# Kernel optimization log

Hardware: AMD Instinct MI355X
Metric: run time of the kernel (lower is better)

Reference implementation:

```python
import jax, jax.numpy as jnp
import numpy as np

GAMMA = 0.5  # triplet_loss_gamma from __init__


def setup_inputs() -> dict:
    key = jax.random.key(0)
    k1, k2, k3 = jax.random.split(key, 3)
    b, n, m = 16, 2048, 2048
    scores = jax.random.normal(k1, (b, n + 1, m + 1), dtype=jnp.float32)
    gt_matches0 = jax.random.randint(k2, (b, n), 0, m, dtype=jnp.int32)
    gt_matches1 = jax.random.randint(k3, (b, m), 0, n, dtype=jnp.int32)
    return {"gt_matches0": gt_matches0, "gt_matches1": gt_matches1, "scores": scores}


def reference(gt_matches0, gt_matches1, scores):
    b, n = gt_matches0.shape
    m = gt_matches1.shape[1]
    # -1 means "unmatched" -> dustbin index (m for rows, n for cols)
    gt0 = jnp.where(gt_matches0 == -1, m, gt_matches0)
    gt1 = jnp.where(gt_matches1 == -1, n, gt_matches1)
    gamma_pos = jnp.maximum(jnp.float32(GAMMA), 0.0)  # clamp value at the matched slot

    # ---- anchor = rows (points in cloud 0) ----
    s0 = scores[:, :n, :]                                   # (b, n, m+1)
    pos0 = jnp.take_along_axis(s0, gt0[:, :, None], axis=2)  # (b, n, 1)
    # original computes -log(exp(pos)) - (-log(exp(neg))) + gamma == neg - pos + gamma
    gap0 = jnp.maximum(s0 - pos0 + GAMMA, 0.0)              # (b, n, m+1)
    # torch version excludes the matched column; its contribution is clamp(gamma, 0)
    sum0 = jnp.sum(gap0, axis=2) - gamma_pos                # (b, n)
    loss_mean = jnp.mean(2.0 * jnp.log(sum0 + 1.0), axis=1)  # (b,)

    # ---- anchor = columns (points in cloud 1) ----
    s1 = scores[:, :, :m]                                   # (b, n+1, m)
    pos1 = jnp.take_along_axis(s1, gt1[:, None, :], axis=1)  # (b, 1, m)
    gap1 = jnp.maximum(s1 - pos1 + GAMMA, 0.0)              # (b, n+1, m)
    sum1 = jnp.sum(gap1, axis=1) - gamma_pos                # (b, m)
    loss_mean2 = jnp.mean(2.0 * jnp.log(sum1 + 1.0), axis=1)  # (b,)

    return (loss_mean + loss_mean2) / 2.0
```

## Files before the change

kernel.cpp:

```cpp
#include <hip/hip_runtime.h>
#include <math.h>

#define BATCH 16
#define NN 2048
#define MM 2048
#define WW 2049
#define RPB 32
#define NCHUNK 65

__global__ __launch_bounds__(256) void gather_kernel(
    const float* __restrict__ scores, const int* __restrict__ gt0,
    const int* __restrict__ gt1, float* __restrict__ pos0, float* __restrict__ pos1)
{
    int id = blockIdx.x * 256 + threadIdx.x;
    const int half = BATCH * NN;
    if (id < half) {
        int b = id >> 11, i = id & (NN - 1);
        int g = gt0[id];
        g = (g == -1) ? MM : g;
        g = min(max(g, 0), MM);
        pos0[id] = scores[(size_t)b * WW * WW + (size_t)i * WW + g];
    } else {
        int id2 = id - half;
        int b = id2 >> 11, j = id2 & (MM - 1);
        int g = gt1[id2];
        g = (g == -1) ? NN : g;
        g = min(max(g, 0), NN);
        pos1[id2] = scores[(size_t)b * WW * WW + (size_t)g * WW + j];
    }
}

__global__ __launch_bounds__(256) void main_kernel(
    const float* __restrict__ scores, const float* __restrict__ pos0,
    const float* __restrict__ pos1, float* __restrict__ colsum,
    float* __restrict__ rowacc)
{
    const int b = blockIdx.y;
    const int row0 = blockIdx.x * RPB;
    const int tid = threadIdx.x;
    const int wave = tid >> 6;
    const int lane = tid & 63;

    const float* sb = scores + (size_t)b * WW * WW;
    const float* p1b = pos1 + b * MM;

    float pos1v[32];
    float colacc[32];
#pragma unroll
    for (int k = 0; k < 32; ++k) {
        pos1v[k] = p1b[lane + 64 * k];
        colacc[k] = 0.0f;
    }

    float rowterm = 0.0f;
    for (int r = wave; r < RPB; r += 4) {
        const int i = row0 + r;
        if (i >= WW) break;
        const bool has_row = (i < NN);
        const float p0 = has_row ? pos0[b * NN + i] : 0.0f;
        const float* rowp = sb + (size_t)i * WW;

        float rowpart = 0.0f;
#pragma unroll
        for (int k = 0; k < 32; ++k) {
            const float s = rowp[lane + 64 * k] + 0.5f;
            rowpart += fmaxf(s - p0, 0.0f);
            colacc[k] += fmaxf(s - pos1v[k], 0.0f);
        }
        if (has_row) {
            if (lane == 0)
                rowpart += fmaxf(rowp[2048] + 0.5f - p0, 0.0f);
#pragma unroll
            for (int off = 32; off; off >>= 1)
                rowpart += __shfl_xor(rowpart, off);
            if (lane == 0)
                rowterm += 2.0f * logf(rowpart + 0.5f);
        }
    }
    if (lane == 0)
        unsafeAtomicAdd(&rowacc[b], rowterm);

    __shared__ float cl[MM];
    for (int j = tid; j < MM; j += 256) cl[j] = 0.0f;
    __syncthreads();
    for (int w = 0; w < 4; ++w) {
        if (wave == w) {
#pragma unroll
            for (int k = 0; k < 32; ++k) cl[lane + 64 * k] += colacc[k];
        }
        __syncthreads();
    }
    for (int j = tid; j < MM; j += 256)
        unsafeAtomicAdd(&colsum[b * MM + j], cl[j]);
}

__global__ __launch_bounds__(256) void finalize_kernel(
    const float* __restrict__ colsum, const float* __restrict__ rowacc,
    float* __restrict__ out)
{
    const int b = blockIdx.x;
    const int tid = threadIdx.x;
    const int wave = tid >> 6;
    const int lane = tid & 63;

    float acc = 0.0f;
    for (int j = tid; j < MM; j += 256)
        acc += 2.0f * logf(colsum[b * MM + j] + 0.5f);

#pragma unroll
    for (int off = 32; off; off >>= 1)
        acc += __shfl_xor(acc, off);

    __shared__ float red[4];
    if (lane == 0) red[wave] = acc;
    __syncthreads();
    if (tid == 0) {
        const float colterms = red[0] + red[1] + red[2] + red[3];
        out[b] = 0.5f * (rowacc[b] * (1.0f / NN) + colterms * (1.0f / MM));
    }
}

extern "C" void kernel_launch(void* const* d_in, const int* in_sizes, int n_in,
                              void* d_out, int out_size, void* d_ws, size_t ws_size,
                              hipStream_t stream) {
    const int* gt0 = (const int*)d_in[0];
    const int* gt1 = (const int*)d_in[1];
    const float* scores = (const float*)d_in[2];
    float* out = (float*)d_out;

    float* ws = (float*)d_ws;
    float* pos0   = ws;
    float* pos1   = ws + (size_t)BATCH * NN;
    float* colsum = ws + (size_t)2 * BATCH * NN;
    float* rowacc = ws + (size_t)3 * BATCH * NN;

    hipMemsetAsync(colsum, 0, ((size_t)BATCH * MM + BATCH) * sizeof(float), stream);

    gather_kernel<<<(2 * BATCH * NN) / 256, 256, 0, stream>>>(scores, gt0, gt1, pos0, pos1);

    dim3 grid(NCHUNK, BATCH);
    main_kernel<<<grid, 256, 0, stream>>>(scores, pos0, pos1, colsum, rowacc);

    finalize_kernel<<<BATCH, 256, 0, stream>>>(colsum, rowacc, out);
}
```

Baseline: 404.4 us.

## Rewrite hinge sums as max(s,q) with offset correction and simplify block reduction

Uses the identity max(s - p + g, 0) = max(s, p - g) - (p - g), so the inner loop becomes a single max and add per element. The gather now stores p - gamma, and the constant offset of 2049*q is subtracted once per row or column at the end. The grid drops from 65 to 64 blocks, with the last block taking 33 rows. The shared-memory column reduction now writes per-wave arrays and sums them with one sync instead of four serialized passes. Subtracting a large offset from a large sum in fp32 risks cancellation error.

```diff
diff --git a/kernel.cpp b/kernel.cpp
--- a/kernel.cpp
+++ b/kernel.cpp
@@ -5,12 +5,11 @@
 #define NN 2048
 #define MM 2048
 #define WW 2049
-#define RPB 32
-#define NCHUNK 65
+#define GAMMA 0.5f
 
 __global__ __launch_bounds__(256) void gather_kernel(
     const float* __restrict__ scores, const int* __restrict__ gt0,
-    const int* __restrict__ gt1, float* __restrict__ pos0, float* __restrict__ pos1)
+    const int* __restrict__ gt1, float* __restrict__ q0, float* __restrict__ q1)
 {
     int id = blockIdx.x * 256 + threadIdx.x;
     const int half = BATCH * NN;
@@ -19,84 +18,81 @@
         int g = gt0[id];
         g = (g == -1) ? MM : g;
         g = min(max(g, 0), MM);
-        pos0[id] = scores[(size_t)b * WW * WW + (size_t)i * WW + g];
+        q0[id] = scores[(size_t)b * WW * WW + (size_t)i * WW + g] - GAMMA;
     } else {
         int id2 = id - half;
         int b = id2 >> 11, j = id2 & (MM - 1);
         int g = gt1[id2];
         g = (g == -1) ? NN : g;
         g = min(max(g, 0), NN);
-        pos1[id2] = scores[(size_t)b * WW * WW + (size_t)g * WW + j];
+        q1[id2] = scores[(size_t)b * WW * WW + (size_t)g * WW + j] - GAMMA;
     }
 }
 
 __global__ __launch_bounds__(256) void main_kernel(
-    const float* __restrict__ scores, const float* __restrict__ pos0,
-    const float* __restrict__ pos1, float* __restrict__ colsum,
+    const float* __restrict__ scores, const float* __restrict__ q0,
+    const float* __restrict__ q1, float* __restrict__ colsum,
     float* __restrict__ rowacc)
 {
     const int b = blockIdx.y;
-    const int row0 = blockIdx.x * RPB;
+    const int row0 = blockIdx.x * 32;
+    const int nrows = (blockIdx.x == 63) ? 33 : 32;
     const int tid = threadIdx.x;
     const int wave = tid >> 6;
     const int lane = tid & 63;
 
     const float* sb = scores + (size_t)b * WW * WW;
-    const float* p1b = pos1 + b * MM;
+    const float* q1b = q1 + b * MM;
 
-    float pos1v[32];
+    float q1v[32];
     float colacc[32];
 #pragma unroll
     for (int k = 0; k < 32; ++k) {
-        pos1v[k] = p1b[lane + 64 * k];
+        q1v[k] = q1b[lane + 64 * k];
         colacc[k] = 0.0f;
     }
 
     float rowterm = 0.0f;
-    for (int r = wave; r < RPB; r += 4) {
+    for (int r = wave; r < nrows; r += 4) {
         const int i = row0 + r;
-        if (i >= WW) break;
         const bool has_row = (i < NN);
-        const float p0 = has_row ? pos0[b * NN + i] : 0.0f;
+        const float q0i = has_row ? q0[b * NN + i] : 0.0f;
         const float* rowp = sb + (size_t)i * WW;
 
-        float rowpart = 0.0f;
+        float rp = 0.0f;
 #pragma unroll
         for (int k = 0; k < 32; ++k) {
-            const float s = rowp[lane + 64 * k] + 0.5f;
-            rowpart += fmaxf(s - p0, 0.0f);
-            colacc[k] += fmaxf(s - pos1v[k], 0.0f);
+            const float s = rowp[lane + 64 * k];
+            rp += fmaxf(s, q0i);
+            colacc[k] = fmaxf(s, q1v[k]) + colacc[k];
         }
         if (has_row) {
             if (lane == 0)
-                rowpart += fmaxf(rowp[2048] + 0.5f - p0, 0.0f);
+                rp += fmaxf(rowp[2048], q0i);
 #pragma unroll
             for (int off = 32; off; off >>= 1)
-                rowpart += __shfl_xor(rowpart, off);
+                rp += __shfl_xor(rp, off);
             if (lane == 0)
-                rowterm += 2.0f * logf(rowpart + 0.5f);
+                rowterm += 2.0f * logf(rp - 2049.0f * q0i + 0.5f);
         }
     }
     if (lane == 0)
         unsafeAtomicAdd(&rowacc[b], rowterm);
 
-    __shared__ float cl[MM];
-    for (int j = tid; j < MM; j += 256) cl[j] = 0.0f;
+    __shared__ float cl[4][MM];
+#pragma unroll
+    for (int k = 0; k < 32; ++k)
+        cl[wave][lane + 64 * k] = colacc[k];
     __syncthreads();
-    for (int w = 0; w < 4; ++w) {
-        if (wave == w) {
-#pragma unroll
-            for (int k = 0; k < 32; ++k) cl[lane + 64 * k] += colacc[k];
-        }
-        __syncthreads();
+    for (int j = tid; j < MM; j += 256) {
+        const float v = cl[0][j] + cl[1][j] + cl[2][j] + cl[3][j];
+        unsafeAtomicAdd(&colsum[b * MM + j], v);
     }
-    for (int j = tid; j < MM; j += 256)
-        unsafeAtomicAdd(&colsum[b * MM + j], cl[j]);
 }
 
 __global__ __launch_bounds__(256) void finalize_kernel(
-    const float* __restrict__ colsum, const float* __restrict__ rowacc,
-    float* __restrict__ out)
+    const float* __restrict__ colsum, const float* __restrict__ q1,
+    const float* __restrict__ rowacc, float* __restrict__ out)
 {
     const int b = blockIdx.x;
     const int tid = threadIdx.x;
@@ -104,8 +100,10 @@
     const int lane = tid & 63;
 
     float acc = 0.0f;
-    for (int j = tid; j < MM; j += 256)
-        acc += 2.0f * logf(colsum[b * MM + j] + 0.5f);
+    for (int j = tid; j < MM; j += 256) {
+        const float cs = colsum[b * MM + j] - 2049.0f * q1[b * MM + j];
+        acc += 2.0f * logf(cs + 0.5f);
+    }
 
 #pragma unroll
     for (int off = 32; off; off >>= 1)
@@ -129,17 +127,17 @@
     float* out = (float*)d_out;
 
     float* ws = (float*)d_ws;
-    float* pos0   = ws;
-    float* pos1   = ws + (size_t)BATCH * NN;
+    float* q0     = ws;
+    float* q1     = ws + (size_t)BATCH * NN;
     float* colsum = ws + (size_t)2 * BATCH * NN;
     float* rowacc = ws + (size_t)3 * BATCH * NN;
 
     hipMemsetAsync(colsum, 0, ((size_t)BATCH * MM + BATCH) * sizeof(float), stream);
 
-    gather_kernel<<<(2 * BATCH * NN) / 256, 256, 0, stream>>>(scores, gt0, gt1, pos0, pos1);
+    gather_kernel<<<(2 * BATCH * NN) / 256, 256, 0, stream>>>(scores, gt0, gt1, q0, q1);
 
-    dim3 grid(NCHUNK, BATCH);
-    main_kernel<<<grid, 256, 0, stream>>>(scores, pos0, pos1, colsum, rowacc);
+    dim3 grid(64, BATCH);
+    main_kernel<<<grid, 256, 0, stream>>>(scores, q0, q1, colsum, rowacc);
 
-    finalize_kernel<<<BATCH, 256, 0, stream>>>(colsum, rowacc, out);
+    finalize_kernel<<<BATCH, 256, 0, stream>>>(colsum, q1, rowacc, out);
 }
```

Result: faster. 392.1 us (-3.0%).
